# Performance work log

Measured on AMD Instinct MI355X. Metric: run time of the kernel, lower is better.

Reference implementation:

```python
import jax, jax.numpy as jnp
import numpy as np

N_DYADIC = 0   # dyadic refinement order (init kwarg n)
SOLVER = 0     # first-order explicit finite-difference scheme (init kwarg solver)


def _solve_goursat(inc):
    """Solve Goursat PDE K_{p+1,q+1} = K_{p+1,q} + K_{p,q+1} - K_{p,q} + inc[p,q]*K_{p,q}
    with boundary K[0,:] = K[:,0] = 1. inc: [B, P, Q] -> returns K[P,Q] per pair: [B]."""
    B, P, Q = inc.shape
    dt = inc.dtype
    ones_b = jnp.ones((B,), dt)

    def row_step(prev_row, inc_row):
        # prev_row: [B, Q+1] = K[p, :]; inc_row: [B, Q]
        def col_step(k_left, t):
            k_diag, k_up, a = t  # K[p,q], K[p,q+1], inc[p,q], each [B]
            k_new = k_up + (k_left - k_diag) + a * k_diag
            return k_new, k_new
        xs = (prev_row[:, :-1].T, prev_row[:, 1:].T, inc_row.T)  # [Q, B] each
        _, tail = jax.lax.scan(col_step, ones_b, xs)              # tail: [Q, B]
        new_row = jnp.concatenate([ones_b[:, None], tail.T], axis=1)
        return new_row, None

    final_row, _ = jax.lax.scan(row_step, jnp.ones((B, Q + 1), dt), jnp.swapaxes(inc, 0, 1))
    return final_row[:, -1]


def _sig_kernel_gram(X, Y, n=N_DYADIC):
    """Signature-kernel Gram matrix. X: [A, M, D], Y: [B, N, D] -> [A, B]."""
    dX = X[:, 1:, :] - X[:, :-1, :]          # [A, M-1, D]
    dY = Y[:, 1:, :] - Y[:, :-1, :]          # [B, N-1, D]
    Minc = jnp.einsum('apd,bqd->abpq', dX, dY)  # pairwise increment inner products
    f = 2 ** n
    if f > 1:  # dyadic grid refinement: split each cell into f*f subcells
        Minc = jnp.repeat(jnp.repeat(Minc, f, axis=2), f, axis=3) / (f * f)
    A, B, P, Q = Minc.shape
    K = _solve_goursat(Minc.reshape(A * B, P, Q))
    return K.reshape(A, B)


def setup_inputs() -> dict:
    key = jax.random.key(0)
    kx, ky = jax.random.split(key)
    SCALE = 0.05  # small Brownian-like increments keep the exponential kernel tame
    X = jnp.cumsum(SCALE * jax.random.normal(kx, (64, 128, 64), dtype=jnp.float32), axis=1)
    Y = jnp.cumsum(SCALE * jax.random.normal(ky, (64, 128, 64), dtype=jnp.float32), axis=1)
    return {"X": X, "Y": Y}


def reference(X, Y):
    K_XX = _sig_kernel_gram(X, X)
    K_YY = _sig_kernel_gram(Y, Y)
    K_XY = _sig_kernel_gram(X, Y)
    dist = jnp.mean(K_XX) + jnp.mean(K_YY) - 2.0 * jnp.mean(K_XY)
    return jnp.mean((X[:, 0, :] - Y[:, 0, :]) ** 2) + dist
```

## Files before the change

kernel.cpp:

```cpp
#include <hip/hip_runtime.h>
#include <math.h>

#define DD 64
#define MM 128
#define RS 133
#define OD 66
#define P1 2128

typedef float  f32x4v __attribute__((ext_vector_type(4)));
typedef __bf16 bf16x8 __attribute__((ext_vector_type(8)));

#define FOR8(F) F(0) F(1) F(2) F(3) F(4) F(5) F(6) F(7)

union FragU { unsigned int u[4]; bf16x8 v; };

__device__ __forceinline__ unsigned cvtpk(float lo, float hi) {
    unsigned r;
    asm("v_cvt_pk_bf16_f32 %0, %1, %2" : "=v"(r) : "v"(lo), "v"(hi));
    return r;
}

__device__ __forceinline__ bf16x8 dfrag_hi(const float* __restrict__ r0,
                                           const float* __restrict__ r1) {
    float4 a0 = *(const float4*)r0, a1 = *(const float4*)(r0 + 4);
    float4 b0 = *(const float4*)r1, b1 = *(const float4*)(r1 + 4);
    FragU f;
    f.u[0] = cvtpk(b0.x - a0.x, b0.y - a0.y);
    f.u[1] = cvtpk(b0.z - a0.z, b0.w - a0.w);
    f.u[2] = cvtpk(b1.x - a1.x, b1.y - a1.y);
    f.u[3] = cvtpk(b1.z - a1.z, b1.w - a1.w);
    return f.v;
}

template<int CTRL, int RM, bool BC>
__device__ __forceinline__ float dpp_add(float x) {
    int t = __builtin_amdgcn_update_dpp(0, __float_as_int(x), CTRL, RM, 0xf, BC);
    return x + __int_as_float(t);
}
__device__ __forceinline__ float wave_incl_scan(float x) {
    x = dpp_add<0x111, 0xf, true >(x);
    x = dpp_add<0x112, 0xf, true >(x);
    x = dpp_add<0x114, 0xf, true >(x);
    x = dpp_add<0x118, 0xf, true >(x);
    x = dpp_add<0x142, 0xa, false>(x);
    x = dpp_add<0x143, 0xc, false>(x);
    return x;
}

__global__ __launch_bounds__(64, 2) void sig_goursat_kernel(
        const float* __restrict__ X, const float* __restrict__ Y,
        float* __restrict__ Kout)
{
    const int bid = blockIdx.x;
    int g, a0, a1, bcol;
    bool dup = false;
    if (bid < 2112) {
        g = bid < 1056 ? 0 : 1;
        const int t = bid - g * 1056;
        bcol = (int)(2.0f * sqrtf((float)t + 1.0f));
        if (bcol > 63) bcol = 63;
        while (bcol > 0  && ((bcol + 1) * (bcol + 1)) / 4 > t) --bcol;
        while (bcol < 63 && ((bcol + 2) * (bcol + 2)) / 4 <= t) ++bcol;
        const int j = t - ((bcol + 1) * (bcol + 1)) / 4;
        a0 = 2 * j; a1 = 2 * j + 1;
        if (a1 > bcol) { a1 = a0; dup = true; }
    } else {
        const int t = bid - 2112;
        g = 2; bcol = t & 63;
        a0 = (t >> 6) * 2; a1 = a0 + 1;
    }

    const float* __restrict__ Ub = (g == 1 ? Y : X);
    const float* __restrict__ U0 = Ub + (size_t)a0 * (MM * DD);
    const float* __restrict__ U1 = Ub + (size_t)a1 * (MM * DD);
    const float* __restrict__ V  = (g == 0 ? X : Y) + (size_t)bcol * (MM * DD);

    const int lane = threadIdx.x;
    const int l15  = lane & 15;
    const int k8   = (lane >> 4) * 8;
    const int rowg = (lane >> 4) * 4;

    __shared__ float incL[2 * P1];

#define TBDECL(ct) bf16x8 tb0_##ct, tb1_##ct;
    FOR8(TBDECL)
#define TBUILD(ct) { int brow_ = ct * 16 + l15; if (brow_ > 126) brow_ = 126; \
        const float* vp_ = V + (size_t)brow_ * DD + k8; \
        tb0_##ct = dfrag_hi(vp_,      vp_ + DD); \
        tb1_##ct = dfrag_hi(vp_ + 32, vp_ + DD + 32); }
    FOR8(TBUILD)

    float s0e = 1.0f, s0o = 1.0f;
    float s1e = 1.0f, s1o = 1.0f;
    const int wbase = rowg * RS + ((l15 & 1) ? OD : 0) + (l15 >> 1);

#define CTSTEP2(ct) { \
        f32x4v c0 = {0.f, 0.f, 0.f, 0.f}, c1 = {0.f, 0.f, 0.f, 0.f}; \
        c0 = __builtin_amdgcn_mfma_f32_16x16x32_bf16(a0k0, tb0_##ct, c0, 0, 0, 0); \
        c1 = __builtin_amdgcn_mfma_f32_16x16x32_bf16(a1k0, tb0_##ct, c1, 0, 0, 0); \
        c0 = __builtin_amdgcn_mfma_f32_16x16x32_bf16(a0k1, tb1_##ct, c0, 0, 0, 0); \
        c1 = __builtin_amdgcn_mfma_f32_16x16x32_bf16(a1k1, tb1_##ct, c1, 0, 0, 0); \
        const int w_ = wbase + ct * 8; \
        incL[w_]             = c0[0]; \
        incL[w_ + RS]        = c0[1]; \
        incL[w_ + 2*RS]      = c0[2]; \
        incL[w_ + 3*RS]      = c0[3]; \
        incL[P1 + w_]        = c1[0]; \
        incL[P1 + w_ + RS]   = c1[1]; \
        incL[P1 + w_ + 2*RS] = c1[2]; \
        incL[P1 + w_ + 3*RS] = c1[3]; }

#define SCANROW2(r) { \
        const float iE0 = incL[(r) * RS + lane]; \
        const float iO0 = incL[(r) * RS + OD + lane]; \
        const float iE1 = incL[P1 + (r) * RS + lane]; \
        const float iO1 = incL[P1 + (r) * RS + OD + lane]; \
        const float m0a = iE0 * s0e; \
        const float m1a = iO0 * s0o; \
        const float m0b = iE1 * s1e; \
        const float m1b = iO1 * s1o; \
        const float ta  = m0a + m1a; \
        const float tb  = m0b + m1b; \
        const float Sa  = wave_incl_scan(ta); \
        const float Sb  = wave_incl_scan(tb); \
        const float exa = Sa - ta; \
        const float exb = Sb - tb; \
        s0o += exa + m0a;  s0e += exa; \
        s1o += exb + m0b;  s1e += exb; }

    for (int band = 0; band < 8; ++band) {
        int arow = band * 16 + l15; if (arow > 126) arow = 126;
        const float* ap0 = U0 + (size_t)arow * DD + k8;
        const float* ap1 = U1 + (size_t)arow * DD + k8;
        bf16x8 a0k0 = dfrag_hi(ap0,      ap0 + DD);
        bf16x8 a0k1 = dfrag_hi(ap0 + 32, ap0 + DD + 32);
        bf16x8 a1k0 = dfrag_hi(ap1,      ap1 + DD);
        bf16x8 a1k1 = dfrag_hi(ap1 + 32, ap1 + DD + 32);

        FOR8(CTSTEP2)

        #pragma unroll
        for (int r = 0; r < 15; ++r) { SCANROW2(r) }
        if (band < 7) { SCANROW2(15) }
    }

    if (lane == 63) {
        float* kg = Kout + (size_t)g * 4096;
        kg[a0 * 64 + bcol] = s0o;
        if (!dup) kg[a1 * 64 + bcol] = s1o;
    }
}

__global__ void sig_reduce_kernel(const float* __restrict__ X,
                                  const float* __restrict__ Y,
                                  const float* __restrict__ Kws,
                                  float* __restrict__ out)
{
    const int t = threadIdx.x;
    double accK = 0.0, acc2 = 0.0;
    for (int i = t; i < 4096; i += 256) {
        const int a = i >> 6, b = i & 63;
        if (a <= b) {
            const double w = (a == b) ? 1.0 : 2.0;
            accK += w * (double)Kws[i];
            accK += w * (double)Kws[4096 + i];
        }
        accK -= 2.0 * (double)Kws[8192 + i];
        const float df = X[(size_t)a * (MM * DD) + b] - Y[(size_t)a * (MM * DD) + b];
        acc2 += (double)df * (double)df;
    }
    __shared__ double red[256];
    red[t] = accK / 4096.0 + acc2 / 4096.0;
    __syncthreads();
    for (int s = 128; s > 0; s >>= 1) {
        if (t < s) red[t] += red[t + s];
        __syncthreads();
    }
    if (t == 0) out[0] = (float)red[0];
}

extern "C" void kernel_launch(void* const* d_in, const int* in_sizes, int n_in,
                              void* d_out, int out_size, void* d_ws, size_t ws_size,
                              hipStream_t stream) {
    const float* X = (const float*)d_in[0];
    const float* Y = (const float*)d_in[1];
    float* Kws = (float*)d_ws;
    float* out = (float*)d_out;

    sig_goursat_kernel<<<dim3(4160), dim3(64), 0, stream>>>(X, Y, Kws);
    sig_reduce_kernel<<<dim3(1), dim3(256), 0, stream>>>(X, Y, Kws, out);
}
```

Measured before the change: 125.4 us.

## Use natural LDS layout with float2 reads, prefetch scan rows, raise occupancy

Changes the shared-memory increment layout from a split even/odd arrangement to a natural row layout with stride 132, so each lane reads its two adjacent columns with one float2 load instead of two scalar loads. Adds a two-deep software prefetch of the next rows' LDS values ahead of the serial scan, and raises the launch-bounds occupancy hint from 2 to 3 waves. This aims to shorten LDS latency on the serial dependency chain, at the cost of possible store bank conflicts from the MFMA write pattern and more register pressure under the tighter occupancy bound.

```diff
diff --git a/kernel.cpp b/kernel.cpp
--- a/kernel.cpp
+++ b/kernel.cpp
@@ -3,9 +3,9 @@
 
 #define DD 64
 #define MM 128
-#define RS 133
-#define OD 66
-#define P1 2128
+#define RSW 132
+#define P1W 2112
+#define RS2 66
 
 typedef float  f32x4v __attribute__((ext_vector_type(4)));
 typedef __bf16 bf16x8 __attribute__((ext_vector_type(8)));
@@ -47,7 +47,7 @@
     return x;
 }
 
-__global__ __launch_bounds__(64, 2) void sig_goursat_kernel(
+__global__ __launch_bounds__(64, 3) void sig_goursat_kernel(
         const float* __restrict__ X, const float* __restrict__ Y,
         float* __restrict__ Kout)
 {
@@ -80,7 +80,7 @@
     const int k8   = (lane >> 4) * 8;
     const int rowg = (lane >> 4) * 4;
 
-    __shared__ float incL[2 * P1];
+    __shared__ float incL[2 * P1W];
 
 #define TBDECL(ct) bf16x8 tb0_##ct, tb1_##ct;
     FOR8(TBDECL)
@@ -92,7 +92,7 @@
 
     float s0e = 1.0f, s0o = 1.0f;
     float s1e = 1.0f, s1o = 1.0f;
-    const int wbase = rowg * RS + ((l15 & 1) ? OD : 0) + (l15 >> 1);
+    const int wbase = rowg * RSW + l15;
 
 #define CTSTEP2(ct) { \
         f32x4v c0 = {0.f, 0.f, 0.f, 0.f}, c1 = {0.f, 0.f, 0.f, 0.f}; \
@@ -100,25 +100,21 @@
         c1 = __builtin_amdgcn_mfma_f32_16x16x32_bf16(a1k0, tb0_##ct, c1, 0, 0, 0); \
         c0 = __builtin_amdgcn_mfma_f32_16x16x32_bf16(a0k1, tb1_##ct, c0, 0, 0, 0); \
         c1 = __builtin_amdgcn_mfma_f32_16x16x32_bf16(a1k1, tb1_##ct, c1, 0, 0, 0); \
-        const int w_ = wbase + ct * 8; \
-        incL[w_]             = c0[0]; \
-        incL[w_ + RS]        = c0[1]; \
-        incL[w_ + 2*RS]      = c0[2]; \
-        incL[w_ + 3*RS]      = c0[3]; \
-        incL[P1 + w_]        = c1[0]; \
-        incL[P1 + w_ + RS]   = c1[1]; \
-        incL[P1 + w_ + 2*RS] = c1[2]; \
-        incL[P1 + w_ + 3*RS] = c1[3]; }
+        const int w_ = wbase + ct * 16; \
+        incL[w_]              = c0[0]; \
+        incL[w_ + RSW]        = c0[1]; \
+        incL[w_ + 2*RSW]      = c0[2]; \
+        incL[w_ + 3*RSW]      = c0[3]; \
+        incL[P1W + w_]        = c1[0]; \
+        incL[P1W + w_ + RSW]  = c1[1]; \
+        incL[P1W + w_ + 2*RSW]= c1[2]; \
+        incL[P1W + w_ + 3*RSW]= c1[3]; }
 
-#define SCANROW2(r) { \
-        const float iE0 = incL[(r) * RS + lane]; \
-        const float iO0 = incL[(r) * RS + OD + lane]; \
-        const float iE1 = incL[P1 + (r) * RS + lane]; \
-        const float iO1 = incL[P1 + (r) * RS + OD + lane]; \
-        const float m0a = iE0 * s0e; \
-        const float m1a = iO0 * s0o; \
-        const float m0b = iE1 * s1e; \
-        const float m1b = iO1 * s1o; \
+#define SCANROW2C(e0, e1) { \
+        const float m0a = e0.x * s0e; \
+        const float m1a = e0.y * s0o; \
+        const float m0b = e1.x * s1e; \
+        const float m1b = e1.y * s1o; \
         const float ta  = m0a + m1a; \
         const float tb  = m0b + m1b; \
         const float Sa  = wave_incl_scan(ta); \
@@ -127,6 +123,9 @@
         const float exb = Sb - tb; \
         s0o += exa + m0a;  s0e += exa; \
         s1o += exb + m0b;  s1e += exb; }
+
+    const float2* pl0 = (const float2*)&incL[2 * lane];
+    const float2* pl1 = (const float2*)&incL[P1W + 2 * lane];
 
     for (int band = 0; band < 8; ++band) {
         int arow = band * 16 + l15; if (arow > 126) arow = 126;
@@ -139,9 +138,17 @@
 
         FOR8(CTSTEP2)
 
+        float2 e0 = pl0[0],   e1 = pl1[0];
+        float2 f0 = pl0[RS2], f1 = pl1[RS2];
         #pragma unroll
-        for (int r = 0; r < 15; ++r) { SCANROW2(r) }
-        if (band < 7) { SCANROW2(15) }
+        for (int r = 0; r < 14; ++r) {
+            float2 n0 = pl0[(r + 2) * RS2];
+            float2 n1 = pl1[(r + 2) * RS2];
+            SCANROW2C(e0, e1)
+            e0 = f0; e1 = f1; f0 = n0; f1 = n1;
+        }
+        SCANROW2C(e0, e1)
+        if (band < 7) { SCANROW2C(f0, f1) }
     }
 
     if (lane == 63) {
```

Measured after the change: 114.2 us. 1.1x faster.
